# Optimization experiments

Hardware: AMD Instinct MI355X
Metric: run time of the kernel (lower is better)

Reference implementation:

```python
import jax, jax.numpy as jnp
import numpy as np


def _squash(s):
    # s: [B, 10, 16]; norms reduce over the capsule-class dim (axis=1), as in torch code
    s_l2 = jnp.linalg.norm(s, axis=1)[:, :, None]   # [B, 16, 1]
    s_l1 = jnp.sum(jnp.abs(s), axis=1)[:, :, None]  # [B, 16, 1]
    return s_l2 / (1.0 + s_l2) * (jnp.swapaxes(s, 1, 2) / s_l1)  # [B, 16, 10]


def setup_inputs() -> dict:
    key = jax.random.key(0)
    ks = jax.random.split(key, 8)
    B = 1024
    x = jax.random.normal(ks[0], (B, 1, 28, 28), dtype=jnp.float32)
    conv1_w = jax.random.normal(ks[1], (256, 1, 9, 9), dtype=jnp.float32) * 0.05
    conv1_b = jnp.zeros((256,), dtype=jnp.float32)
    prim_w = jax.random.normal(ks[2], (32, 32, 1, 9, 9), dtype=jnp.float32) * 0.05
    prim_b = jnp.zeros((32,), dtype=jnp.float32)
    a = float(np.sqrt(6.0 / (8 + 16)))  # xavier-uniform bound for dig_W
    dig_W = jax.random.uniform(ks[3], (1152, 8, 16), jnp.float32, -a, a)
    dig_Wb = jnp.zeros((1152, 16), dtype=jnp.float32)
    out_w = jax.random.normal(ks[4], (10, 10, 16, 1), dtype=jnp.float32) * 0.05
    out_b = jnp.zeros((10,), dtype=jnp.float32)
    return dict(x=x, conv1_w=conv1_w, conv1_b=conv1_b, prim_w=prim_w, prim_b=prim_b,
                dig_W=dig_W, dig_Wb=dig_Wb, out_w=out_w, out_b=out_b)


def reference(x, conv1_w, conv1_b, prim_w, prim_b, dig_W, dig_Wb, out_w, out_b):
    # conv1: [B,1,28,28] -> [B,256,20,20]
    out = jax.lax.conv_general_dilated(
        x, conv1_w, window_strides=(1, 1), padding='VALID',
        dimension_numbers=('NCHW', 'OIHW', 'NCHW')) + conv1_b[None, :, None, None]
    out = jax.nn.relu(out)
    B = out.shape[0]
    out1 = out.reshape(B, 32, 8, 20, 20)
    # prim_layer Conv3d(32,32,[1,9,9],stride=[1,2,2]): -> [B,32,8,6,6]
    out1 = jax.lax.conv_general_dilated(
        out1, prim_w, window_strides=(1, 2, 2), padding='VALID',
        dimension_numbers=('NCDHW', 'OIDHW', 'NCDHW')) + prim_b[None, :, None, None, None]
    out1 = jax.nn.relu(out1)
    out1 = jnp.swapaxes(out1, 2, 4)        # [B,32,6,6,8]
    out1 = out1.reshape(B, 1152, 8)        # primary capsules
    # per-capsule affine: [B,1152,8] x [1152,8,16] -> [B,1152,16]
    u = jnp.einsum('bne,nef->bnf', out1, dig_W) + dig_Wb
    # dynamic routing, 3 iterations
    b = jnp.zeros((B, 10, 1152), dtype=u.dtype)
    v = None
    for _ in range(3):
        c = jax.nn.softmax(b, axis=1)                       # softmax over 10 classes
        s = jnp.einsum('bjn,bnf->bjf', c, u)                # [B,10,16]
        v = _squash(s)                                      # [B,16,10]
        b = b + jnp.swapaxes(jnp.matmul(u, v), 1, 2)        # [B,10,1152]
    # output conv2d(10,10,[16,1]) on [B,10,16,1] == einsum over (class-in, pose)
    logits = jnp.einsum('bif,oif->bo', jnp.swapaxes(v, 1, 2), out_w[..., 0]) + out_b
    return jax.nn.softmax(logits, axis=1)
```

## Files before the change

kernel.cpp:

```cpp
#include <hip/hip_runtime.h>
#include <math.h>

typedef __attribute__((ext_vector_type(8))) short bf16x8;
typedef __attribute__((ext_vector_type(4))) float f32x4;
#define MFMA16(a, b, c) __builtin_amdgcn_mfma_f32_16x16x32_bf16(a, b, c, 0, 0, 0)

union U8 { bf16x8 v; int i4[4]; };

__device__ __forceinline__ unsigned short f2bf(float x) {
    unsigned u = __builtin_bit_cast(unsigned, x);
    unsigned r = (u + 0x7fffu + ((u >> 16) & 1u)) >> 16;
    return (unsigned short)r;
}
__device__ __forceinline__ unsigned cvtpk(float lo, float hi) {
    unsigned r;
    asm("v_cvt_pk_bf16_f32 %0, %1, %2" : "=v"(r) : "v"(lo), "v"(hi));
    return r;
}

__device__ __forceinline__ int koff_of(int kidx) {
    int grp = kidx >> 3, e = kidx & 7;
    if (grp < 9)  return grp * 9 + e;
    if (grp == 9) return e * 9 + 8;
    if (grp == 10) return (e == 0) ? 80 : -1;
    return -1;
}

#define CAPS_BYTES 37748736
#define A1F_ELEMS  24576
#define W3F_ELEMS  82944

__global__ void k_prep(const float* __restrict__ c1w,
                       const float* __restrict__ pw,
                       unsigned short* __restrict__ w1f,
                       unsigned short* __restrict__ w3f)
{
    int idx = blockIdx.x * 256 + threadIdx.x;
    if (idx < A1F_ELEMS) {
        int e = idx & 7, lane = (idx >> 3) & 63, f = idx >> 9;
        int k3 = f % 3, m = (f / 3) & 1, d = f / 6;
        int ch = (lane & 15) + m * 16;
        int kidx = k3 * 32 + ((lane >> 4) << 3) + e;
        int ko = koff_of(kidx);
        w1f[idx] = f2bf(ko >= 0 ? c1w[(ch * 8 + d) * 81 + ko] : 0.f);
    } else if (idx < A1F_ELEMS + W3F_ELEMS) {
        int j = idx - A1F_ELEMS;
        int e = j & 7, lane = (j >> 3) & 63, f = j >> 9;
        int m = f & 1, tap = f >> 1;
        int oc = (lane & 15) + m * 16;
        int i = ((lane >> 4) << 3) + e;
        w3f[j] = f2bf(pw[oc * 2592 + i * 81 + tap]);
    }
}

__global__ __launch_bounds__(256, 4) void k_conv(
    const float* __restrict__ x,
    const float* __restrict__ c1b,
    const float* __restrict__ pb,
    const unsigned short* __restrict__ w1f,
    const unsigned short* __restrict__ w3f,
    float* __restrict__ caps)
{
    __shared__ __align__(16) unsigned short img[800];
    __shared__ __align__(16) unsigned short imgs[800];
    __shared__ __align__(128) unsigned short interm[400 * 40];

    const int t = threadIdx.x;
    const int lane = t & 63, w = t >> 6;
    const int g = lane >> 4, col = lane & 15;
    const int b = blockIdx.x >> 3, d = blockIdx.x & 7;

    for (int idx = t; idx < 784; idx += 256) {
        unsigned short v = f2bf(x[b * 784 + idx]);
        img[idx] = v;
        if (idx > 0) imgs[idx - 1] = v;
    }
    __syncthreads();

    {
        bf16x8 a1[2][3];
        const bf16x8* w1p = (const bf16x8*)w1f;
#pragma unroll
        for (int m = 0; m < 2; ++m)
#pragma unroll
            for (int k3 = 0; k3 < 3; ++k3)
                a1[m][k3] = w1p[((d * 2 + m) * 3 + k3) * 64 + lane];

        float bias[2][4];
#pragma unroll
        for (int m = 0; m < 2; ++m)
#pragma unroll
            for (int r = 0; r < 4; ++r)
                bias[m][r] = c1b[(m * 16 + g * 4 + r) * 8 + d];

        for (int q = w; q < 25; q += 4) {
            int p = q * 16 + col;
            int py = p / 20, px = p - py * 20;
            int base = py * 28 + px;
            const unsigned short* rbase = (base & 1) ? &imgs[base - 1] : &img[base];

            bf16x8 bfrag[3];
#pragma unroll
            for (int k3 = 0; k3 < 2; ++k3) {
                int grp = k3 * 4 + g;
                U8 u8;
#pragma unroll
                for (int qq = 0; qq < 4; ++qq)
                    u8.i4[qq] = *(const int*)(rbase + grp * 28 + 2 * qq);
                bfrag[k3] = u8.v;
            }
            {
                U8 u8;
                if (g == 0) {
#pragma unroll
                    for (int qq = 0; qq < 4; ++qq)
                        u8.i4[qq] = *(const int*)(rbase + 8 * 28 + 2 * qq);
                } else if (g == 1) {
#pragma unroll
                    for (int e = 0; e < 8; ++e)
                        u8.v[e] = (short)img[base + e * 28 + 8];
                } else if (g == 2) {
                    u8.i4[0] = u8.i4[1] = u8.i4[2] = u8.i4[3] = 0;
                    u8.v[0] = (short)img[base + 8 * 28 + 8];
                } else {
                    u8.i4[0] = u8.i4[1] = u8.i4[2] = u8.i4[3] = 0;
                }
                bfrag[2] = u8.v;
            }

            f32x4 acc0 = {0.f, 0.f, 0.f, 0.f};
            f32x4 acc1 = {0.f, 0.f, 0.f, 0.f};
#pragma unroll
            for (int k3 = 0; k3 < 3; ++k3) {
                acc0 = MFMA16(a1[0][k3], bfrag[k3], acc0);
                acc1 = MFMA16(a1[1][k3], bfrag[k3], acc1);
            }
            float r0[4], r1[4];
#pragma unroll
            for (int r = 0; r < 4; ++r) {
                r0[r] = fmaxf(acc0[r] + bias[0][r], 0.f);
                r1[r] = fmaxf(acc1[r] + bias[1][r], 0.f);
            }
            *(uint2*)(&interm[p * 40 + g * 4])      = make_uint2(cvtpk(r0[0], r0[1]), cvtpk(r0[2], r0[3]));
            *(uint2*)(&interm[p * 40 + 16 + g * 4]) = make_uint2(cvtpk(r1[0], r1[1]), cvtpk(r1[2], r1[3]));
        }
    }
    __syncthreads();

    f32x4 acc[2][3];
#pragma unroll
    for (int m = 0; m < 2; ++m)
#pragma unroll
        for (int nt = 0; nt < 3; ++nt)
            acc[m][nt] = (f32x4){0.f, 0.f, 0.f, 0.f};
    {
        int abase[3];
#pragma unroll
        for (int nt = 0; nt < 3; ++nt) {
            int p2 = nt * 16 + col;
            int xw = p2 / 6, yh = p2 - xw * 6;
            int pos0 = (p2 < 36) ? (yh * 40 + xw * 2) : 0;
            abase[nt] = pos0 * 80 + g * 16;
        }
        const bf16x8* w3p = (const bf16x8*)w3f;
        const char* ib = (const char*)interm;

        for (int rr = 0; rr < 2; ++rr) {
            const int ky = 2 * w + rr;
            const bf16x8* wrow = w3p + (ky * 9) * 128;
            const char* B0 = ib + abase[0] + ky * 1600;
            const char* B1 = ib + abase[1] + ky * 1600;
            const char* B2 = ib + abase[2] + ky * 1600;
#pragma unroll
            for (int kx = 0; kx < 9; ++kx) {
                bf16x8 a0  = wrow[kx * 128 + lane];
                bf16x8 a1v = wrow[kx * 128 + 64 + lane];
                bf16x8 b0 = *(const bf16x8*)(B0 + kx * 80);
                bf16x8 b1 = *(const bf16x8*)(B1 + kx * 80);
                bf16x8 b2 = *(const bf16x8*)(B2 + kx * 80);
                acc[0][0] = MFMA16(a0, b0, acc[0][0]);
                acc[1][0] = MFMA16(a1v, b0, acc[1][0]);
                acc[0][1] = MFMA16(a0, b1, acc[0][1]);
                acc[1][1] = MFMA16(a1v, b1, acc[1][1]);
                acc[0][2] = MFMA16(a0, b2, acc[0][2]);
                acc[1][2] = MFMA16(a1v, b2, acc[1][2]);
            }
        }
        {
            const bf16x8* wrow = w3p + 72 * 128;
            const char* B0 = ib + abase[0] + 12800;
            const char* B1 = ib + abase[1] + 12800;
            const char* B2 = ib + abase[2] + 12800;
            int kx0 = 2 * w;
            int nkx = (w == 3) ? 3 : 2;
#pragma unroll 3
            for (int q = 0; q < nkx; ++q) {
                int kx = kx0 + q;
                bf16x8 a0  = wrow[kx * 128 + lane];
                bf16x8 a1v = wrow[kx * 128 + 64 + lane];
                bf16x8 b0 = *(const bf16x8*)(B0 + kx * 80);
                bf16x8 b1 = *(const bf16x8*)(B1 + kx * 80);
                bf16x8 b2 = *(const bf16x8*)(B2 + kx * 80);
                acc[0][0] = MFMA16(a0, b0, acc[0][0]);
                acc[1][0] = MFMA16(a1v, b0, acc[1][0]);
                acc[0][1] = MFMA16(a0, b1, acc[0][1]);
                acc[1][1] = MFMA16(a1v, b1, acc[1][1]);
                acc[0][2] = MFMA16(a0, b2, acc[0][2]);
                acc[1][2] = MFMA16(a1v, b2, acc[1][2]);
            }
        }
    }
    __syncthreads();
    f32x4* rp = (f32x4*)&interm[0];
    {
#pragma unroll
        for (int m = 0; m < 2; ++m)
#pragma unroll
            for (int nt = 0; nt < 3; ++nt)
                rp[(w * 6 + m * 3 + nt) * 64 + lane] = acc[m][nt];
    }
    __syncthreads();
    for (int idx = t; idx < 384; idx += 256) {
        int tile = idx >> 6, ls = idx & 63;
        f32x4 s = rp[tile * 64 + ls];
#pragma unroll
        for (int ww = 1; ww < 4; ++ww)
            s += rp[(ww * 6 + tile) * 64 + ls];
        int m = tile / 3, nt = tile - m * 3;
        int p2 = nt * 16 + (ls & 15);
        if (p2 < 36) {
            int gr = ls >> 4;
#pragma unroll
            for (int r = 0; r < 4; ++r) {
                int oc = m * 16 + gr * 4 + r;
                caps[(b * 8 + d) * 1152 + oc * 36 + p2] = fmaxf(s[r] + pb[oc], 0.f);
            }
        }
    }
}

#define USB 1160
#define CSB 1160

__global__ __launch_bounds__(576, 5) void k_route(
    const float* __restrict__ caps,
    const float* __restrict__ W,
    const float* __restrict__ Wb,
    const float* __restrict__ ow,
    const float* __restrict__ ob,
    float* __restrict__ out)
{
    __shared__ __align__(16) unsigned short u_bf[16 * USB];
    __shared__ __align__(16) unsigned short c_bf[10 * CSB];
    __shared__ __align__(16) float sred[9 * 256];
    __shared__ __align__(16) float vv[16 * 12];
    __shared__ float ss[160];
    __shared__ float red2[16];

    const int t = threadIdx.x;
    const int lane = t & 63, wv = t >> 6;
    const int g = lane >> 4, col = lane & 15;
    const int b = blockIdx.x;
    const int n0 = 2 * t;

    {
        const int nl = t >> 2, fq = t & 3;
        for (int base = 0; base < 1152; base += 144) {
            int n = base + nl;
            float cv[8];
#pragma unroll
            for (int e = 0; e < 8; ++e) cv[e] = caps[(b * 8 + e) * 1152 + n];
            float4 a4 = ((const float4*)(Wb + n * 16))[fq];
#pragma unroll
            for (int e = 0; e < 8; ++e) {
                float4 w4 = ((const float4*)(W + n * 128 + e * 16))[fq];
                a4.x += cv[e] * w4.x; a4.y += cv[e] * w4.y;
                a4.z += cv[e] * w4.z; a4.w += cv[e] * w4.w;
            }
            u_bf[(fq * 4 + 0) * USB + n] = f2bf(a4.x);
            u_bf[(fq * 4 + 1) * USB + n] = f2bf(a4.y);
            u_bf[(fq * 4 + 2) * USB + n] = f2bf(a4.z);
            u_bf[(fq * 4 + 3) * USB + n] = f2bf(a4.w);
        }
    }
    float breg[2][10];
#pragma unroll
    for (int s = 0; s < 2; ++s)
#pragma unroll
        for (int jj = 0; jj < 10; ++jj) breg[s][jj] = 0.f;
    __syncthreads();

    const int jrow = (col < 10) ? col : 9;

    for (int iter = 0; iter < 3; ++iter) {
        {
            float cv2[2][10];
#pragma unroll
            for (int s = 0; s < 2; ++s) {
                float m = breg[s][0];
#pragma unroll
                for (int jj = 1; jj < 10; ++jj) m = fmaxf(m, breg[s][jj]);
                float sum = 0.f;
#pragma unroll
                for (int jj = 0; jj < 10; ++jj) { cv2[s][jj] = __expf(breg[s][jj] - m); sum += cv2[s][jj]; }
                float inv = 1.f / sum;
#pragma unroll
                for (int jj = 0; jj < 10; ++jj) cv2[s][jj] *= inv;
            }
#pragma unroll
            for (int jj = 0; jj < 10; ++jj)
                *(unsigned*)(&c_bf[jj * CSB + n0]) = cvtpk(cv2[0][jj], cv2[1][jj]);
        }
        __syncthreads();
        {
            f32x4 sp = {0.f, 0.f, 0.f, 0.f};
#pragma unroll
            for (int mf = 0; mf < 4; ++mf) {
                int nk = wv * 128 + mf * 32 + g * 8;
                bf16x8 af = *(const bf16x8*)(&c_bf[jrow * CSB + nk]);
                bf16x8 bf = *(const bf16x8*)(&u_bf[col * USB + nk]);
                sp = MFMA16(af, bf, sp);
            }
            *(f32x4*)(&sred[wv * 256 + lane * 4]) = sp;
        }
        __syncthreads();
        if (t < 160) {
            int j = t >> 4, f = t & 15;
            int li = ((j >> 2) * 16 + f) * 4 + (j & 3);
            float s = 0.f;
#pragma unroll
            for (int ww = 0; ww < 9; ++ww) s += sred[ww * 256 + li];
            ss[j * 16 + f] = s;
        }
        __syncthreads();
        if (t < 16) {
            float sv[10], l2 = 0.f, l1 = 0.f;
#pragma unroll
            for (int jj = 0; jj < 10; ++jj) {
                sv[jj] = ss[jj * 16 + t];
                l2 += sv[jj] * sv[jj]; l1 += fabsf(sv[jj]);
            }
            l2 = sqrtf(l2);
            float scale = l2 / (1.f + l2) / l1;
#pragma unroll
            for (int jj = 0; jj < 10; ++jj) vv[t * 12 + jj] = sv[jj] * scale;
        }
        __syncthreads();
        if (iter < 2) {
#pragma unroll
            for (int f = 0; f < 16; ++f) {
                unsigned pair = *(const unsigned*)(&u_bf[f * USB + n0]);
                float ux = __builtin_bit_cast(float, pair << 16);
                float uy = __builtin_bit_cast(float, pair & 0xffff0000u);
                f32x4 v0 = *(const f32x4*)(&vv[f * 12]);
                f32x4 v1 = *(const f32x4*)(&vv[f * 12 + 4]);
                float2 v2 = *(const float2*)(&vv[f * 12 + 8]);
                breg[0][0] += ux * v0.x; breg[1][0] += uy * v0.x;
                breg[0][1] += ux * v0.y; breg[1][1] += uy * v0.y;
                breg[0][2] += ux * v0.z; breg[1][2] += uy * v0.z;
                breg[0][3] += ux * v0.w; breg[1][3] += uy * v0.w;
                breg[0][4] += ux * v1.x; breg[1][4] += uy * v1.x;
                breg[0][5] += ux * v1.y; breg[1][5] += uy * v1.y;
                breg[0][6] += ux * v1.z; breg[1][6] += uy * v1.z;
                breg[0][7] += ux * v1.w; breg[1][7] += uy * v1.w;
                breg[0][8] += ux * v2.x; breg[1][8] += uy * v2.x;
                breg[0][9] += ux * v2.y; breg[1][9] += uy * v2.y;
            }
        }
        __syncthreads();
    }

    if (t < 10) {
        float l = ob[t];
#pragma unroll
        for (int i2 = 0; i2 < 10; ++i2)
#pragma unroll
            for (int ff = 0; ff < 16; ++ff)
                l += vv[ff * 12 + i2] * ow[t * 160 + i2 * 16 + ff];
        red2[t] = l;
    }
    __syncthreads();
    if (t == 0) {
        float m = -1e30f;
        for (int o = 0; o < 10; ++o) m = fmaxf(m, red2[o]);
        float sum = 0.f; float e[10];
        for (int o = 0; o < 10; ++o) { e[o] = __expf(red2[o] - m); sum += e[o]; }
        float inv = 1.f / sum;
        for (int o = 0; o < 10; ++o) out[b * 10 + o] = e[o] * inv;
    }
}

extern "C" void kernel_launch(void* const* d_in, const int* in_sizes, int n_in,
                              void* d_out, int out_size, void* d_ws, size_t ws_size,
                              hipStream_t stream) {
    const float* x     = (const float*)d_in[0];
    const float* c1w   = (const float*)d_in[1];
    const float* c1b   = (const float*)d_in[2];
    const float* pw    = (const float*)d_in[3];
    const float* pb    = (const float*)d_in[4];
    const float* digW  = (const float*)d_in[5];
    const float* digWb = (const float*)d_in[6];
    const float* outw  = (const float*)d_in[7];
    const float* outb  = (const float*)d_in[8];
    float* out = (float*)d_out;

    float* caps = (float*)d_ws;
    unsigned short* w1f = (unsigned short*)((char*)d_ws + CAPS_BYTES);
    unsigned short* w3f = w1f + A1F_ELEMS;

    k_prep<<<dim3(420), dim3(256), 0, stream>>>(c1w, pw, w1f, w3f);
    k_conv<<<dim3(8192), dim3(256), 0, stream>>>(x, c1b, pb, w1f, w3f, caps);
    k_route<<<dim3(1024), dim3(576), 0, stream>>>(caps, digW, digWb, outw, outb, out);
}
```

Measured before the change: 181.5 us.

## Store conv1 output phase-split for stride-2 conv and use bf16 digit weights

The conv1 output tile in shared memory is now stored in a polyphase (even/odd row and column) layout, so the stride-2 primary-capsule conv reads contiguous rows via a small offset table. The output spatial index mapping changes accordingly, with the transpose moved into the caps store. The digit-capsule weight matrix is also pre-converted to bf16 in the prep kernel, which halves the weight bytes read per block in the routing kernel. This adds a larger prep launch and bf16 rounding of the affine weights, and leaves a stray no-op statement in the routing kernel.

```diff
diff --git a/kernel.cpp b/kernel.cpp
--- a/kernel.cpp
+++ b/kernel.cpp
@@ -29,11 +29,14 @@
 #define CAPS_BYTES 37748736
 #define A1F_ELEMS  24576
 #define W3F_ELEMS  82944
+#define WBF_ELEMS  147456
 
 __global__ void k_prep(const float* __restrict__ c1w,
                        const float* __restrict__ pw,
+                       const float* __restrict__ digW,
                        unsigned short* __restrict__ w1f,
-                       unsigned short* __restrict__ w3f)
+                       unsigned short* __restrict__ w3f,
+                       unsigned short* __restrict__ wbf)
 {
     int idx = blockIdx.x * 256 + threadIdx.x;
     if (idx < A1F_ELEMS) {
@@ -50,6 +53,9 @@
         int oc = (lane & 15) + m * 16;
         int i = ((lane >> 4) << 3) + e;
         w3f[j] = f2bf(pw[oc * 2592 + i * 81 + tap]);
+    } else if (idx < A1F_ELEMS + W3F_ELEMS + WBF_ELEMS) {
+        int j = idx - A1F_ELEMS - W3F_ELEMS;
+        wbf[j] = f2bf(digW[j]);
     }
 }
 
@@ -141,8 +147,11 @@
                 r0[r] = fmaxf(acc0[r] + bias[0][r], 0.f);
                 r1[r] = fmaxf(acc1[r] + bias[1][r], 0.f);
             }
-            *(uint2*)(&interm[p * 40 + g * 4])      = make_uint2(cvtpk(r0[0], r0[1]), cvtpk(r0[2], r0[3]));
-            *(uint2*)(&interm[p * 40 + 16 + g * 4]) = make_uint2(cvtpk(r1[0], r1[1]), cvtpk(r1[2], r1[3]));
+            int rr2 = (py & 1) * 10 + (py >> 1);
+            int cc2 = (px & 1) * 10 + (px >> 1);
+            int sidx = rr2 * 20 + cc2;
+            *(uint2*)(&interm[sidx * 40 + g * 4])      = make_uint2(cvtpk(r0[0], r0[1]), cvtpk(r0[2], r0[3]));
+            *(uint2*)(&interm[sidx * 40 + 16 + g * 4]) = make_uint2(cvtpk(r1[0], r1[1]), cvtpk(r1[2], r1[3]));
         }
     }
     __syncthreads();
@@ -154,30 +163,32 @@
         for (int nt = 0; nt < 3; ++nt)
             acc[m][nt] = (f32x4){0.f, 0.f, 0.f, 0.f};
     {
+        const int KOFF[9] = {0, 800, 80, 880, 160, 960, 240, 1040, 320};
         int abase[3];
 #pragma unroll
         for (int nt = 0; nt < 3; ++nt) {
             int p2 = nt * 16 + col;
-            int xw = p2 / 6, yh = p2 - xw * 6;
-            int pos0 = (p2 < 36) ? (yh * 40 + xw * 2) : 0;
-            abase[nt] = pos0 * 80 + g * 16;
+            int xw, yh;
+            if (p2 < 36) { yh = p2 / 6; xw = p2 - yh * 6; } else { yh = 0; xw = 0; }
+            abase[nt] = (yh * 20 + xw) * 80 + g * 16;
         }
         const bf16x8* w3p = (const bf16x8*)w3f;
         const char* ib = (const char*)interm;
 
         for (int rr = 0; rr < 2; ++rr) {
             const int ky = 2 * w + rr;
+            const int roff = (rr == 0) ? (w * 1600) : ((10 + w) * 1600);
             const bf16x8* wrow = w3p + (ky * 9) * 128;
-            const char* B0 = ib + abase[0] + ky * 1600;
-            const char* B1 = ib + abase[1] + ky * 1600;
-            const char* B2 = ib + abase[2] + ky * 1600;
+            const char* B0 = ib + abase[0] + roff;
+            const char* B1 = ib + abase[1] + roff;
+            const char* B2 = ib + abase[2] + roff;
 #pragma unroll
             for (int kx = 0; kx < 9; ++kx) {
                 bf16x8 a0  = wrow[kx * 128 + lane];
                 bf16x8 a1v = wrow[kx * 128 + 64 + lane];
-                bf16x8 b0 = *(const bf16x8*)(B0 + kx * 80);
-                bf16x8 b1 = *(const bf16x8*)(B1 + kx * 80);
-                bf16x8 b2 = *(const bf16x8*)(B2 + kx * 80);
+                bf16x8 b0 = *(const bf16x8*)(B0 + KOFF[kx]);
+                bf16x8 b1 = *(const bf16x8*)(B1 + KOFF[kx]);
+                bf16x8 b2 = *(const bf16x8*)(B2 + KOFF[kx]);
                 acc[0][0] = MFMA16(a0, b0, acc[0][0]);
                 acc[1][0] = MFMA16(a1v, b0, acc[1][0]);
                 acc[0][1] = MFMA16(a0, b1, acc[0][1]);
@@ -188,9 +199,9 @@
         }
         {
             const bf16x8* wrow = w3p + 72 * 128;
-            const char* B0 = ib + abase[0] + 12800;
-            const char* B1 = ib + abase[1] + 12800;
-            const char* B2 = ib + abase[2] + 12800;
+            const char* B0 = ib + abase[0] + 6400;
+            const char* B1 = ib + abase[1] + 6400;
+            const char* B2 = ib + abase[2] + 6400;
             int kx0 = 2 * w;
             int nkx = (w == 3) ? 3 : 2;
 #pragma unroll 3
@@ -198,9 +209,9 @@
                 int kx = kx0 + q;
                 bf16x8 a0  = wrow[kx * 128 + lane];
                 bf16x8 a1v = wrow[kx * 128 + 64 + lane];
-                bf16x8 b0 = *(const bf16x8*)(B0 + kx * 80);
-                bf16x8 b1 = *(const bf16x8*)(B1 + kx * 80);
-                bf16x8 b2 = *(const bf16x8*)(B2 + kx * 80);
+                bf16x8 b0 = *(const bf16x8*)(B0 + KOFF[kx]);
+                bf16x8 b1 = *(const bf16x8*)(B1 + KOFF[kx]);
+                bf16x8 b2 = *(const bf16x8*)(B2 + KOFF[kx]);
                 acc[0][0] = MFMA16(a0, b0, acc[0][0]);
                 acc[1][0] = MFMA16(a1v, b0, acc[1][0]);
                 acc[0][1] = MFMA16(a0, b1, acc[0][1]);
@@ -229,11 +240,12 @@
         int m = tile / 3, nt = tile - m * 3;
         int p2 = nt * 16 + (ls & 15);
         if (p2 < 36) {
+            int yh = p2 / 6, xw = p2 - yh * 6;
             int gr = ls >> 4;
 #pragma unroll
             for (int r = 0; r < 4; ++r) {
                 int oc = m * 16 + gr * 4 + r;
-                caps[(b * 8 + d) * 1152 + oc * 36 + p2] = fmaxf(s[r] + pb[oc], 0.f);
+                caps[(b * 8 + d) * 1152 + oc * 36 + xw * 6 + yh] = fmaxf(s[r] + pb[oc], 0.f);
             }
         }
     }
@@ -244,7 +256,7 @@
 
 __global__ __launch_bounds__(576, 5) void k_route(
     const float* __restrict__ caps,
-    const float* __restrict__ W,
+    const unsigned short* __restrict__ Wbf,
     const float* __restrict__ Wb,
     const float* __restrict__ ow,
     const float* __restrict__ ob,
@@ -273,10 +285,15 @@
             float4 a4 = ((const float4*)(Wb + n * 16))[fq];
 #pragma unroll
             for (int e = 0; e < 8; ++e) {
-                float4 w4 = ((const float4*)(W + n * 128 + e * 16))[fq];
-                a4.x += cv[e] * w4.x; a4.y += cv[e] * w4.y;
-                a4.z += cv[e] * w4.z; a4.w += cv[e] * w4.w;
-            }
+                uint2 wp = *(const uint2*)(&Wbf[n * 128 + e * 16 + fq * 4]);
+                float w0 = __builtin_bit_cast(float, wp.x << 16);
+                float w1 = __builtin_bit_cast(float, wp.x & 0xffff0000u);
+                float w2 = __builtin_bit_cast(float, wp.y << 16);
+                float w3 = __builtin_bit_cast(float, wp.y & 0xffff0000u);
+                a4.x += cv[e] * w0; a4.y += cv[e] * w1;
+                a4.z += cv[e] * w2; a4.w += cv[e] * w3;
+            }
+            *(unsigned*)(&u_bf[(fq * 4 + 0) * USB + n]) ;
             u_bf[(fq * 4 + 0) * USB + n] = f2bf(a4.x);
             u_bf[(fq * 4 + 1) * USB + n] = f2bf(a4.y);
             u_bf[(fq * 4 + 2) * USB + n] = f2bf(a4.z);
@@ -407,8 +424,9 @@
     float* caps = (float*)d_ws;
     unsigned short* w1f = (unsigned short*)((char*)d_ws + CAPS_BYTES);
     unsigned short* w3f = w1f + A1F_ELEMS;
-
-    k_prep<<<dim3(420), dim3(256), 0, stream>>>(c1w, pw, w1f, w3f);
+    unsigned short* wbf = w3f + W3F_ELEMS;
+
+    k_prep<<<dim3(996), dim3(256), 0, stream>>>(c1w, pw, digW, w1f, w3f, wbf);
     k_conv<<<dim3(8192), dim3(256), 0, stream>>>(x, c1b, pb, w1f, w3f, caps);
-    k_route<<<dim3(1024), dim3(576), 0, stream>>>(caps, digW, digWb, outw, outb, out);
-}
+    k_route<<<dim3(1024), dim3(576), 0, stream>>>(caps, wbf, digWb, outw, outb, out);
+}
```

New measurement: 178.3 us. No clear change (-1.8%).

## Shrink routing LDS footprint with half-split coefficient staging and bf16 dig weights

Applied to the files above, without the earlier changes.

The routing kernel now stages the softmax coefficients in two halves through a smaller shared buffer, reusing it as the reduction scratch. This removes the separate sred array so more blocks fit per CU, and the launch-bounds hint is raised accordingly. The per-capsule weight matrix is converted to bf16 in the prep kernel, halving the bytes each routing block reads. The price is two extra barriers per iteration and a slight loss of precision in the weights.

```diff
diff --git a/kernel.cpp b/kernel.cpp
--- a/kernel.cpp
+++ b/kernel.cpp
@@ -29,11 +29,14 @@
 #define CAPS_BYTES 37748736
 #define A1F_ELEMS  24576
 #define W3F_ELEMS  82944
+#define WBF_ELEMS  147456
 
 __global__ void k_prep(const float* __restrict__ c1w,
                        const float* __restrict__ pw,
+                       const float* __restrict__ digW,
                        unsigned short* __restrict__ w1f,
-                       unsigned short* __restrict__ w3f)
+                       unsigned short* __restrict__ w3f,
+                       unsigned short* __restrict__ wbf)
 {
     int idx = blockIdx.x * 256 + threadIdx.x;
     if (idx < A1F_ELEMS) {
@@ -50,6 +53,9 @@
         int oc = (lane & 15) + m * 16;
         int i = ((lane >> 4) << 3) + e;
         w3f[j] = f2bf(pw[oc * 2592 + i * 81 + tap]);
+    } else if (idx < A1F_ELEMS + W3F_ELEMS + WBF_ELEMS) {
+        int j = idx - A1F_ELEMS - W3F_ELEMS;
+        wbf[j] = f2bf(digW[j]);
     }
 }
 
@@ -240,19 +246,18 @@
 }
 
 #define USB 1160
-#define CSB 1160
-
-__global__ __launch_bounds__(576, 5) void k_route(
+#define CHS 584
+
+__global__ __launch_bounds__(576, 8) void k_route(
     const float* __restrict__ caps,
-    const float* __restrict__ W,
+    const unsigned short* __restrict__ Wbf,
     const float* __restrict__ Wb,
     const float* __restrict__ ow,
     const float* __restrict__ ob,
     float* __restrict__ out)
 {
     __shared__ __align__(16) unsigned short u_bf[16 * USB];
-    __shared__ __align__(16) unsigned short c_bf[10 * CSB];
-    __shared__ __align__(16) float sred[9 * 256];
+    __shared__ __align__(16) unsigned short chalf[10 * CHS];
     __shared__ __align__(16) float vv[16 * 12];
     __shared__ float ss[160];
     __shared__ float red2[16];
@@ -273,9 +278,13 @@
             float4 a4 = ((const float4*)(Wb + n * 16))[fq];
 #pragma unroll
             for (int e = 0; e < 8; ++e) {
-                float4 w4 = ((const float4*)(W + n * 128 + e * 16))[fq];
-                a4.x += cv[e] * w4.x; a4.y += cv[e] * w4.y;
-                a4.z += cv[e] * w4.z; a4.w += cv[e] * w4.w;
+                uint2 wp = *(const uint2*)(&Wbf[n * 128 + e * 16 + fq * 4]);
+                float w0 = __builtin_bit_cast(float, wp.x << 16);
+                float w1 = __builtin_bit_cast(float, wp.x & 0xffff0000u);
+                float w2 = __builtin_bit_cast(float, wp.y << 16);
+                float w3 = __builtin_bit_cast(float, wp.y & 0xffff0000u);
+                a4.x += cv[e] * w0; a4.y += cv[e] * w1;
+                a4.z += cv[e] * w2; a4.w += cv[e] * w3;
             }
             u_bf[(fq * 4 + 0) * USB + n] = f2bf(a4.x);
             u_bf[(fq * 4 + 1) * USB + n] = f2bf(a4.y);
@@ -291,8 +300,11 @@
     __syncthreads();
 
     const int jrow = (col < 10) ? col : 9;
+    const int hmine = (t >= 288);
+    const int nh = 2 * t - 576 * hmine;
 
     for (int iter = 0; iter < 3; ++iter) {
+        unsigned pk[10];
         {
             float cv2[2][10];
 #pragma unroll
@@ -309,27 +321,36 @@
             }
 #pragma unroll
             for (int jj = 0; jj < 10; ++jj)
-                *(unsigned*)(&c_bf[jj * CSB + n0]) = cvtpk(cv2[0][jj], cv2[1][jj]);
-        }
-        __syncthreads();
-        {
-            f32x4 sp = {0.f, 0.f, 0.f, 0.f};
-#pragma unroll
-            for (int mf = 0; mf < 4; ++mf) {
-                int nk = wv * 128 + mf * 32 + g * 8;
-                bf16x8 af = *(const bf16x8*)(&c_bf[jrow * CSB + nk]);
-                bf16x8 bf = *(const bf16x8*)(&u_bf[col * USB + nk]);
+                pk[jj] = cvtpk(cv2[0][jj], cv2[1][jj]);
+        }
+
+        f32x4 sp = {0.f, 0.f, 0.f, 0.f};
+#pragma unroll
+        for (int h = 0; h < 2; ++h) {
+            if (hmine == h) {
+#pragma unroll
+                for (int jj = 0; jj < 10; ++jj)
+                    *(unsigned*)(&chalf[jj * CHS + nh]) = pk[jj];
+            }
+            __syncthreads();
+#pragma unroll
+            for (int mf = 0; mf < 2; ++mf) {
+                int nk = wv * 64 + mf * 32 + g * 8;
+                bf16x8 af = *(const bf16x8*)(&chalf[jrow * CHS + nk]);
+                bf16x8 bf = *(const bf16x8*)(&u_bf[col * USB + h * 576 + nk]);
                 sp = MFMA16(af, bf, sp);
             }
-            *(f32x4*)(&sred[wv * 256 + lane * 4]) = sp;
-        }
+            __syncthreads();
+        }
+        float* scratch = (float*)chalf;
+        *(f32x4*)(&scratch[(wv * 64 + lane) * 4]) = sp;
         __syncthreads();
         if (t < 160) {
             int j = t >> 4, f = t & 15;
             int li = ((j >> 2) * 16 + f) * 4 + (j & 3);
             float s = 0.f;
 #pragma unroll
-            for (int ww = 0; ww < 9; ++ww) s += sred[ww * 256 + li];
+            for (int ww = 0; ww < 9; ++ww) s += scratch[ww * 256 + li];
             ss[j * 16 + f] = s;
         }
         __syncthreads();
@@ -407,8 +428,9 @@
     float* caps = (float*)d_ws;
     unsigned short* w1f = (unsigned short*)((char*)d_ws + CAPS_BYTES);
     unsigned short* w3f = w1f + A1F_ELEMS;
-
-    k_prep<<<dim3(420), dim3(256), 0, stream>>>(c1w, pw, w1f, w3f);
+    unsigned short* wbf = w3f + W3F_ELEMS;
+
+    k_prep<<<dim3(996), dim3(256), 0, stream>>>(c1w, pw, digW, w1f, w3f, wbf);
     k_conv<<<dim3(8192), dim3(256), 0, stream>>>(x, c1b, pb, w1f, w3f, caps);
-    k_route<<<dim3(1024), dim3(576), 0, stream>>>(caps, digW, digWb, outw, outb, out);
-}
+    k_route<<<dim3(1024), dim3(576), 0, stream>>>(caps, wbf, digWb, outw, outb, out);
+}
```

Measured after the change: 169.2 us. 6.8% less time.
